# Kernel optimization log

Measured on AMD Instinct MI355X. Metric: run time of the kernel, lower is better.

Reference implementation:

```python
import jax, jax.numpy as jnp
import numpy as np

B, N, H, NH = 2, 2048, 1024, 16
HD = H // NH


def setup_inputs() -> dict:
    key = jax.random.key(0)
    ks = jax.random.split(key, 12)
    s = 0.02
    inp = {
        "q": jax.random.normal(ks[0], (B, N, H), jnp.float32),
        "k": jax.random.normal(ks[1], (B, N, H), jnp.float32),
        "v": jax.random.normal(ks[2], (B, N, H), jnp.float32),
        # causal mask, broadcast over batch and heads
        "mask": jnp.tril(jnp.ones((N, N), jnp.float32))[None, None, :, :],
        "Wq": jax.random.normal(ks[3], (H, H), jnp.float32) * s,
        "bq": jnp.zeros((H,), jnp.float32),
        "Wk": jax.random.normal(ks[4], (H, H), jnp.float32) * s,
        "bk": jnp.zeros((H,), jnp.float32),
        "Wv": jax.random.normal(ks[5], (H, H), jnp.float32) * s,
        "bv": jnp.zeros((H,), jnp.float32),
        "Wp": jax.random.normal(ks[6], (H, H), jnp.float32) * s,
        "bp": jnp.zeros((H,), jnp.float32),
    }
    return inp


def _split_heads(x):
    # [b, n, (h d)] -> [b, h, n, d]
    b, n, _ = x.shape
    return x.reshape(b, n, NH, HD).transpose(0, 2, 1, 3)


def reference(q, k, v, mask, Wq, bq, Wk, bk, Wv, bv, Wp, bp):
    Q = _split_heads(q @ Wq.T + bq)                      # [b,h,n,d]
    K = _split_heads(k @ Wk.T + bk)
    V = _split_heads(v @ Wv.T + bv)
    scores = jnp.einsum("bhnd,bhmd->bhnm", Q, K) / jnp.sqrt(jnp.float32(HD))
    scores = jnp.where(mask == 0, -jnp.inf, scores)
    attn = jax.nn.softmax(scores, axis=-1)
    out = jnp.einsum("bhnm,bhmd->bhnd", attn, V)         # [b,h,n,d]
    out = out.transpose(0, 2, 1, 3).reshape(q.shape[0], q.shape[1], H)
    # dropout is identity in eval mode
    return out @ Wp.T + bp
```

## Files before the change

kernel.cpp:

```cpp
#include <hip/hip_runtime.h>


typedef unsigned short ushortT;
typedef unsigned int uintT;
typedef __attribute__((ext_vector_type(8))) short short8;
typedef __attribute__((ext_vector_type(4))) float f32x4;

#define M_ROWS 4096
#define KDIM   1024
#define NDIM   1024
#define SEQ    2048
#define HDHEAD 64

__device__ __forceinline__ float bf2f(ushortT s) {
    union { unsigned u; float f; } v; v.u = ((unsigned)s) << 16; return v.f;
}
__device__ __forceinline__ ushortT f2bf(float x) {
    union { float f; unsigned u; } v; v.f = x;
    return (ushortT)((v.u + 0x7fffu + ((v.u >> 16) & 1u)) >> 16);
}

__device__ __forceinline__ bool detect_f32(const uintT* w) {
    int hits = 0;
#pragma unroll
    for (int i = 0; i < 16; ++i) {
        const unsigned e = (w[i] >> 7) & 0xffu;
        hits += (e >= 118u && e <= 131u) ? 1 : 0;
    }
    return hits < 8;
}

__device__ __forceinline__ short8 cvt8(const float* p) {
    f32x4 a = *(const f32x4*)p;
    f32x4 b = *(const f32x4*)(p + 4);
    short8 r;
    r[0] = (short)f2bf(a[0]); r[1] = (short)f2bf(a[1]);
    r[2] = (short)f2bf(a[2]); r[3] = (short)f2bf(a[3]);
    r[4] = (short)f2bf(b[0]); r[5] = (short)f2bf(b[1]);
    r[6] = (short)f2bf(b[2]); r[7] = (short)f2bf(b[3]);
    return r;
}

__device__ __forceinline__ void gl2lds16(const ushortT* g, ushortT* l) {
    __builtin_amdgcn_global_load_lds(
        (const __attribute__((address_space(1))) void*)g,
        (__attribute__((address_space(3))) void*)l,
        16, 0, 0);
}

__global__ __launch_bounds__(256) void convert_kernel(
    const void* __restrict__ q, const void* __restrict__ k, const void* __restrict__ v,
    const void* __restrict__ Wq, const void* __restrict__ Wk,
    const void* __restrict__ Wv, const void* __restrict__ Wp,
    const void* __restrict__ bq, const void* __restrict__ bk,
    const void* __restrict__ bv, const void* __restrict__ bp,
    ushortT* __restrict__ dst) {
    const bool f32m = detect_f32((const uintT*)q);
    const size_t u = (size_t)blockIdx.x * 256 + threadIdx.x;

    const void* src; size_t soff, doff;
    if (u < 1572864u) {
        const int seg = (int)(u >> 19);
        const size_t o = u & 524287u;
        src  = seg == 0 ? q : (seg == 1 ? k : v);
        soff = o * 8;
        doff = (size_t)seg * 4194304u + o * 8;
    } else if (u < 2097152u) {
        const size_t u2 = u - 1572864u;
        const int seg = (int)(u2 >> 17);
        const size_t o = u2 & 131071u;
        src  = seg == 0 ? Wq : (seg == 1 ? Wk : (seg == 2 ? Wv : Wp));
        soff = o * 8;
        doff = 12582912u + (size_t)seg * 1048576u + o * 8;
    } else {
        const size_t u3 = u - 2097152u;
        const int seg = (int)(u3 >> 7);
        const size_t o = u3 & 127u;
        src  = seg == 0 ? bq : (seg == 1 ? bk : (seg == 2 ? bv : bp));
        soff = o * 8;
        doff = 16777216u + (size_t)seg * 1024u + o * 8;
    }

    if (f32m)
        *(short8*)(dst + doff) = cvt8((const float*)src + soff);
    else
        *(short8*)(dst + doff) = *(const short8*)((const ushortT*)src + soff);
}

__device__ __forceinline__ void gemm_body(const void* __restrict__ Av,
                                          const void* __restrict__ Wv_,
                                          const void* __restrict__ biasv,
                                          void* __restrict__ Cv,
                                          bool a_f32, bool w_f32, bool c_f32) {
    __shared__ ushortT ldsA[128 * 32];
    __shared__ ushortT ldsB[128 * 32];

    const int tid  = threadIdx.x;
    const int lane = tid & 63;
    const int wid  = tid >> 6;
    const int bm   = blockIdx.x;
    const int bn   = blockIdx.y;
    const int wm   = wid >> 1;
    const int wn   = wid & 1;

    const int srow = lane >> 2;
    const int scol = (lane & 3) * 8;

    f32x4 acc[4][4];
#pragma unroll
    for (int i = 0; i < 4; ++i)
#pragma unroll
        for (int j = 0; j < 4; ++j) acc[i][j] = (f32x4){0.f, 0.f, 0.f, 0.f};

    const int fr   = lane & 15;
    const int quad = lane >> 4;

    for (int kt = 0; kt < KDIM / 32; ++kt) {
        const int k0 = kt * 32;
        if (!a_f32 && !w_f32) {
#pragma unroll
            for (int t = 0; t < 2; ++t) {
                const int chunk = wid * 2 + t;
                const size_t ra = (size_t)(bm * 128 + chunk * 16 + srow) * KDIM + k0 + scol;
                const size_t rw = (size_t)(bn * 128 + chunk * 16 + srow) * KDIM + k0 + scol;
                gl2lds16((const ushortT*)Av + ra, ldsA + chunk * 512);
                gl2lds16((const ushortT*)Wv_ + rw, ldsB + chunk * 512);
            }
        } else {
            short8 ta[2], tb[2];
#pragma unroll
            for (int t = 0; t < 2; ++t) {
                const int chunk = wid * 2 + t;
                const size_t ra = (size_t)(bm * 128 + chunk * 16 + srow) * KDIM + k0 + scol;
                const size_t rw = (size_t)(bn * 128 + chunk * 16 + srow) * KDIM + k0 + scol;
                ta[t] = a_f32 ? cvt8((const float*)Av + ra)
                              : *(const short8*)((const ushortT*)Av + ra);
                tb[t] = w_f32 ? cvt8((const float*)Wv_ + rw)
                              : *(const short8*)((const ushortT*)Wv_ + rw);
            }
#pragma unroll
            for (int t = 0; t < 2; ++t) {
                const int chunk = wid * 2 + t;
                *(short8*)(ldsA + chunk * 512 + lane * 8) = ta[t];
                *(short8*)(ldsB + chunk * 512 + lane * 8) = tb[t];
            }
        }
        __syncthreads();

        short8 aF[4], bF[4];
#pragma unroll
        for (int i = 0; i < 4; ++i)
            aF[i] = *(const short8*)(ldsA + (wm * 64 + i * 16 + fr) * 32 + quad * 8);
#pragma unroll
        for (int j = 0; j < 4; ++j)
            bF[j] = *(const short8*)(ldsB + (wn * 64 + j * 16 + fr) * 32 + quad * 8);
#pragma unroll
        for (int i = 0; i < 4; ++i)
#pragma unroll
            for (int j = 0; j < 4; ++j)
                acc[i][j] = __builtin_amdgcn_mfma_f32_16x16x32_bf16(aF[i], bF[j], acc[i][j], 0, 0, 0);
        __syncthreads();
    }

#pragma unroll
    for (int j = 0; j < 4; ++j) {
        const int col = bn * 128 + wn * 64 + j * 16 + fr;
        const float bv = w_f32 ? ((const float*)biasv)[col]
                               : bf2f(((const ushortT*)biasv)[col]);
#pragma unroll
        for (int i = 0; i < 4; ++i) {
            const int row0 = bm * 128 + wm * 64 + i * 16 + quad * 4;
#pragma unroll
            for (int r = 0; r < 4; ++r) {
                const float val = acc[i][j][r] + bv;
                if (c_f32)
                    ((float*)Cv)[(size_t)(row0 + r) * NDIM + col] = val;
                else
                    ((ushortT*)Cv)[(size_t)(row0 + r) * NDIM + col] = f2bf(val);
            }
        }
    }
}

__global__ __launch_bounds__(256, 2) void qkv_proj_kernel(
    const void* __restrict__ q, const void* __restrict__ k, const void* __restrict__ v,
    const void* __restrict__ Wq, const void* __restrict__ Wk, const void* __restrict__ Wv,
    const void* __restrict__ bq, const void* __restrict__ bk, const void* __restrict__ bv,
    ushortT* __restrict__ Qp, ushortT* __restrict__ Kp, ushortT* __restrict__ Vp) {
    const bool f32m = detect_f32((const uintT*)q);
    const void* A; const void* W; const void* bias; ushortT* C;
    if (blockIdx.z == 0)      { A = q; W = Wq; bias = bq; C = Qp; }
    else if (blockIdx.z == 1) { A = k; W = Wk; bias = bk; C = Kp; }
    else                      { A = v; W = Wv; bias = bv; C = Vp; }
    gemm_body(A, W, bias, (void*)C, f32m, f32m, false);
}

__global__ __launch_bounds__(256, 2) void out_proj_kernel(
    const ushortT* __restrict__ A, const void* __restrict__ W,
    const void* __restrict__ bias, void* __restrict__ C,
    const void* __restrict__ qdet) {
    const bool wf = detect_f32((const uintT*)W);
    const bool cf = detect_f32((const uintT*)qdet);
    gemm_body((const void*)A, W, bias, C, false, wf, cf);
}

__global__ __launch_bounds__(256, 2) void flash_attn_kernel(
    const ushortT* __restrict__ Qp, const ushortT* __restrict__ Kp,
    const ushortT* __restrict__ Vp, ushortT* __restrict__ Op) {
    __shared__ ushortT ldsK[2 * 64 * 40];
    __shared__ ushortT ldsV[64 * 72];
    __shared__ ushortT ldsP[4][16 * 72];

    const int tid  = threadIdx.x;
    const int lane = tid & 63;
    const int wid  = tid >> 6;
    const int fr   = lane & 15;
    const int quad = lane >> 4;

    const int pid = blockIdx.x;
    const int h   = blockIdx.y;
    const int b   = blockIdx.z;

    const size_t base = (size_t)b * SEQ * NDIM + (size_t)h * HDHEAD;
    const float scale = 0.125f;

    int ksst[2], keyloc[2];
#pragma unroll
    for (int t = 0; t < 2; ++t) {
        const int chunk = wid * 2 + t;
        ksst[t]   = chunk >> 2;
        keyloc[t] = (chunk & 3) * 16 + (lane >> 2);
    }
    const int c8 = (lane & 3) * 8;
    const int vj = lane;

    for (int half = 0; half < 2; ++half) {
        const int qb = (half == 0) ? pid : (31 - pid);
        const int q0 = qb * 64;
        const int nkv = qb + 1;

        short8 qf[2];
#pragma unroll
        for (int ks = 0; ks < 2; ++ks)
            qf[ks] = *(const short8*)(Qp + base + (size_t)(q0 + wid * 16 + fr) * NDIM + ks * 32 + quad * 8);

        f32x4 accO[4];
#pragma unroll
        for (int dt = 0; dt < 4; ++dt) accO[dt] = (f32x4){0.f, 0.f, 0.f, 0.f};
        float lsum[4];
#pragma unroll
        for (int r = 0; r < 4; ++r) lsum[r] = 0.f;

        short8 kreg[2], vreg[2];
#pragma unroll
        for (int t = 0; t < 2; ++t) {
            kreg[t] = *(const short8*)(Kp + base + (size_t)keyloc[t] * NDIM + ksst[t] * 32 + c8);
            vreg[t] = *(const short8*)(Vp + base + (size_t)vj * NDIM + (wid + t * 4) * 8);
        }

        for (int kt = 0; kt < nkv; ++kt) {
            __syncthreads();

#pragma unroll
            for (int t = 0; t < 2; ++t)
                *(short8*)(ldsK + ksst[t] * 2560 + keyloc[t] * 40 + c8) = kreg[t];
#pragma unroll
            for (int t = 0; t < 2; ++t) {
                const int d0 = (wid + t * 4) * 8;
                const ushortT* vs = (const ushortT*)&vreg[t];
#pragma unroll
                for (int i = 0; i < 8; ++i)
                    ldsV[(d0 + i) * 72 + vj] = vs[i];
            }

            if (kt + 1 < nkv) {
                const int kv1 = (kt + 1) * 64;
#pragma unroll
                for (int t = 0; t < 2; ++t) {
                    kreg[t] = *(const short8*)(Kp + base + (size_t)(kv1 + keyloc[t]) * NDIM + ksst[t] * 32 + c8);
                    vreg[t] = *(const short8*)(Vp + base + (size_t)(kv1 + vj) * NDIM + (wid + t * 4) * 8);
                }
            }
            __syncthreads();

            f32x4 s[4];
#pragma unroll
            for (int nt = 0; nt < 4; ++nt) {
                f32x4 a = (f32x4){0.f, 0.f, 0.f, 0.f};
#pragma unroll
                for (int ks = 0; ks < 2; ++ks) {
                    short8 kf = *(const short8*)(ldsK + ks * 2560 + (nt * 16 + fr) * 40 + quad * 8);
                    a = __builtin_amdgcn_mfma_f32_16x16x32_bf16(qf[ks], kf, a, 0, 0, 0);
                }
                s[nt] = a;
            }

            const int kv0 = kt * 64;
            const int qi = q0 + wid * 16 + quad * 4;
            if (kt == nkv - 1) {
#pragma unroll
                for (int nt = 0; nt < 4; ++nt) {
                    const int kj = kv0 + nt * 16 + fr;
#pragma unroll
                    for (int r = 0; r < 4; ++r) {
                        float vv = s[nt][r] * scale;
                        s[nt][r] = (kj > qi + r) ? -1e30f : vv;
                    }
                }
            } else {
#pragma unroll
                for (int nt = 0; nt < 4; ++nt)
#pragma unroll
                    for (int r = 0; r < 4; ++r) s[nt][r] *= scale;
            }

            ushortT* pbuf = ldsP[wid];
#pragma unroll
            for (int nt = 0; nt < 4; ++nt) {
#pragma unroll
                for (int r = 0; r < 4; ++r) {
                    const float p = __expf(fminf(s[nt][r], 30.f));
                    lsum[r] += p;
                    pbuf[(quad * 4 + r) * 72 + nt * 16 + fr] = f2bf(p);
                }
            }

            asm volatile("" ::: "memory");

#pragma unroll
            for (int ks = 0; ks < 2; ++ks) {
                short8 pf = *(const short8*)(pbuf + fr * 72 + ks * 32 + quad * 8);
#pragma unroll
                for (int dt = 0; dt < 4; ++dt) {
                    short8 vf = *(const short8*)(ldsV + (dt * 16 + fr) * 72 + ks * 32 + quad * 8);
                    accO[dt] = __builtin_amdgcn_mfma_f32_16x16x32_bf16(pf, vf, accO[dt], 0, 0, 0);
                }
            }
        }

#pragma unroll
        for (int r = 0; r < 4; ++r) {
#pragma unroll
            for (int off = 8; off >= 1; off >>= 1)
                lsum[r] += __shfl_xor(lsum[r], off, 64);
        }
#pragma unroll
        for (int dt = 0; dt < 4; ++dt) {
#pragma unroll
            for (int r = 0; r < 4; ++r) {
                const size_t row = (size_t)(q0 + wid * 16 + quad * 4 + r);
                Op[(size_t)b * SEQ * NDIM + row * NDIM + h * HDHEAD + dt * 16 + fr] =
                    f2bf(accO[dt][r] / lsum[r]);
            }
        }
    }
}

extern "C" void kernel_launch(void* const* d_in, const int* in_sizes, int n_in,
                              void* d_out, int out_size, void* d_ws, size_t ws_size,
                              hipStream_t stream) {
    const void* q  = d_in[0];
    const void* k  = d_in[1];
    const void* v  = d_in[2];
    const void* Wq = d_in[4];
    const void* bq = d_in[5];
    const void* Wk = d_in[6];
    const void* bk = d_in[7];
    const void* Wv = d_in[8];
    const void* bv = d_in[9];
    const void* Wp = d_in[10];
    const void* bp = d_in[11];

    dim3 blk(256);
    const size_t FAST_WS = 58728448;

    if (ws_size >= FAST_WS) {
        ushortT* cb   = (ushortT*)d_ws;
        ushortT* qb16 = cb;
        ushortT* kb16 = cb + 4194304u;
        ushortT* vb16 = cb + 8388608u;
        ushortT* Wqb  = cb + 12582912u;
        ushortT* Wkb  = cb + 13631488u;
        ushortT* Wvb  = cb + 14680064u;
        ushortT* Wpb  = cb + 15728640u;
        ushortT* bqb  = cb + 16777216u;
        ushortT* bkb  = cb + 16778240u;
        ushortT* bvb  = cb + 16779264u;
        ushortT* bpb  = cb + 16780288u;
        ushortT* Qp   = cb + 16781312u;
        ushortT* Kp   = Qp + 4194304u;
        ushortT* Vp   = Kp + 4194304u;
        ushortT* Op   = qb16;

        convert_kernel<<<dim3(8194), blk, 0, stream>>>(
            q, k, v, Wq, Wk, Wv, Wp, bq, bk, bv, bp, cb);
        qkv_proj_kernel<<<dim3(32, 8, 3), blk, 0, stream>>>(
            qb16, kb16, vb16, Wqb, Wkb, Wvb, bqb, bkb, bvb, Qp, Kp, Vp);
        flash_attn_kernel<<<dim3(16, 16, 2), blk, 0, stream>>>(Qp, Kp, Vp, Op);
        out_proj_kernel<<<dim3(32, 8), blk, 0, stream>>>(Op, Wpb, bpb, d_out, q);
    } else {
        ushortT* ws = (ushortT*)d_ws;
        ushortT* Qp = ws;
        ushortT* Kp = ws + (size_t)M_ROWS * NDIM;
        ushortT* Vp = ws + (size_t)2 * M_ROWS * NDIM;
        ushortT* Op = ws + (size_t)3 * M_ROWS * NDIM;

        qkv_proj_kernel<<<dim3(32, 8, 3), blk, 0, stream>>>(
            q, k, v, Wq, Wk, Wv, bq, bk, bv, Qp, Kp, Vp);
        flash_attn_kernel<<<dim3(16, 16, 2), blk, 0, stream>>>(Qp, Kp, Vp, Op);
        out_proj_kernel<<<dim3(32, 8), blk, 0, stream>>>(Op, Wp, bp, d_out, q);
    }
}
```

Measured before the change: 251.9 us.

## Store V transposed from projection, fold softmax scale into Q, deepen GEMM K-tile

The QKV projection now writes V in a head-major transposed layout [b,h,d,n], so the attention kernel can store V tiles into LDS with vector writes instead of eight scalar scatter stores per thread. The 1/sqrt(d) scale is applied in the Q projection epilogue, which removes the per-element multiply in attention. The GEMM K-step doubles to 64, halving the number of barrier pairs per tile. In exchange, the transposed V store is a strided scalar scatter in the projection epilogue, LDS per GEMM block doubles, and scaling Q before bf16 rounding slightly changes numerics.

```diff
diff --git a/kernel.cpp b/kernel.cpp
--- a/kernel.cpp
+++ b/kernel.cpp
@@ -91,9 +91,10 @@
                                           const void* __restrict__ Wv_,
                                           const void* __restrict__ biasv,
                                           void* __restrict__ Cv,
-                                          bool a_f32, bool w_f32, bool c_f32) {
-    __shared__ ushortT ldsA[128 * 32];
-    __shared__ ushortT ldsB[128 * 32];
+                                          bool a_f32, bool w_f32, bool c_f32,
+                                          float cscale, bool vt_store) {
+    __shared__ ushortT ldsA[128 * 64];
+    __shared__ ushortT ldsB[128 * 64];
 
     const int tid  = threadIdx.x;
     const int lane = tid & 63;
@@ -115,50 +116,57 @@
     const int fr   = lane & 15;
     const int quad = lane >> 4;
 
-    for (int kt = 0; kt < KDIM / 32; ++kt) {
-        const int k0 = kt * 32;
+    for (int kt = 0; kt < KDIM / 64; ++kt) {
+        const int k0 = kt * 64;
         if (!a_f32 && !w_f32) {
 #pragma unroll
-            for (int t = 0; t < 2; ++t) {
-                const int chunk = wid * 2 + t;
-                const size_t ra = (size_t)(bm * 128 + chunk * 16 + srow) * KDIM + k0 + scol;
-                const size_t rw = (size_t)(bn * 128 + chunk * 16 + srow) * KDIM + k0 + scol;
+            for (int t = 0; t < 4; ++t) {
+                const int chunk = wid * 4 + t;
+                const int kh  = chunk >> 3;
+                const int r16 = (chunk & 7) * 16;
+                const size_t ra = (size_t)(bm * 128 + r16 + srow) * KDIM + k0 + kh * 32 + scol;
+                const size_t rw = (size_t)(bn * 128 + r16 + srow) * KDIM + k0 + kh * 32 + scol;
                 gl2lds16((const ushortT*)Av + ra, ldsA + chunk * 512);
                 gl2lds16((const ushortT*)Wv_ + rw, ldsB + chunk * 512);
             }
         } else {
-            short8 ta[2], tb[2];
-#pragma unroll
-            for (int t = 0; t < 2; ++t) {
-                const int chunk = wid * 2 + t;
-                const size_t ra = (size_t)(bm * 128 + chunk * 16 + srow) * KDIM + k0 + scol;
-                const size_t rw = (size_t)(bn * 128 + chunk * 16 + srow) * KDIM + k0 + scol;
+            short8 ta[4], tb[4];
+#pragma unroll
+            for (int t = 0; t < 4; ++t) {
+                const int chunk = wid * 4 + t;
+                const int kh  = chunk >> 3;
+                const int r16 = (chunk & 7) * 16;
+                const size_t ra = (size_t)(bm * 128 + r16 + srow) * KDIM + k0 + kh * 32 + scol;
+                const size_t rw = (size_t)(bn * 128 + r16 + srow) * KDIM + k0 + kh * 32 + scol;
                 ta[t] = a_f32 ? cvt8((const float*)Av + ra)
                               : *(const short8*)((const ushortT*)Av + ra);
                 tb[t] = w_f32 ? cvt8((const float*)Wv_ + rw)
                               : *(const short8*)((const ushortT*)Wv_ + rw);
             }
 #pragma unroll
-            for (int t = 0; t < 2; ++t) {
-                const int chunk = wid * 2 + t;
+            for (int t = 0; t < 4; ++t) {
+                const int chunk = wid * 4 + t;
                 *(short8*)(ldsA + chunk * 512 + lane * 8) = ta[t];
                 *(short8*)(ldsB + chunk * 512 + lane * 8) = tb[t];
             }
         }
         __syncthreads();
 
-        short8 aF[4], bF[4];
-#pragma unroll
-        for (int i = 0; i < 4; ++i)
-            aF[i] = *(const short8*)(ldsA + (wm * 64 + i * 16 + fr) * 32 + quad * 8);
-#pragma unroll
-        for (int j = 0; j < 4; ++j)
-            bF[j] = *(const short8*)(ldsB + (wn * 64 + j * 16 + fr) * 32 + quad * 8);
-#pragma unroll
-        for (int i = 0; i < 4; ++i)
+#pragma unroll
+        for (int s = 0; s < 2; ++s) {
+            short8 aF[4], bF[4];
+#pragma unroll
+            for (int i = 0; i < 4; ++i)
+                aF[i] = *(const short8*)(ldsA + s * 4096 + (wm * 64 + i * 16 + fr) * 32 + quad * 8);
 #pragma unroll
             for (int j = 0; j < 4; ++j)
-                acc[i][j] = __builtin_amdgcn_mfma_f32_16x16x32_bf16(aF[i], bF[j], acc[i][j], 0, 0, 0);
+                bF[j] = *(const short8*)(ldsB + s * 4096 + (wn * 64 + j * 16 + fr) * 32 + quad * 8);
+#pragma unroll
+            for (int i = 0; i < 4; ++i)
+#pragma unroll
+                for (int j = 0; j < 4; ++j)
+                    acc[i][j] = __builtin_amdgcn_mfma_f32_16x16x32_bf16(aF[i], bF[j], acc[i][j], 0, 0, 0);
+        }
         __syncthreads();
     }
 
@@ -172,11 +180,17 @@
             const int row0 = bm * 128 + wm * 64 + i * 16 + quad * 4;
 #pragma unroll
             for (int r = 0; r < 4; ++r) {
-                const float val = acc[i][j][r] + bv;
-                if (c_f32)
-                    ((float*)Cv)[(size_t)(row0 + r) * NDIM + col] = val;
-                else
-                    ((ushortT*)Cv)[(size_t)(row0 + r) * NDIM + col] = f2bf(val);
+                const float val = (acc[i][j][r] + bv) * cscale;
+                const int row = row0 + r;
+                if (vt_store) {
+                    const int bb = row >> 11, n = row & 2047;
+                    const int hh = col >> 6,  d = col & 63;
+                    ((ushortT*)Cv)[(size_t)((bb * 16 + hh) * 64 + d) * SEQ + n] = f2bf(val);
+                } else if (c_f32) {
+                    ((float*)Cv)[(size_t)row * NDIM + col] = val;
+                } else {
+                    ((ushortT*)Cv)[(size_t)row * NDIM + col] = f2bf(val);
+                }
             }
         }
     }
@@ -186,13 +200,14 @@
     const void* __restrict__ q, const void* __restrict__ k, const void* __restrict__ v,
     const void* __restrict__ Wq, const void* __restrict__ Wk, const void* __restrict__ Wv,
     const void* __restrict__ bq, const void* __restrict__ bk, const void* __restrict__ bv,
-    ushortT* __restrict__ Qp, ushortT* __restrict__ Kp, ushortT* __restrict__ Vp) {
+    ushortT* __restrict__ Qp, ushortT* __restrict__ Kp, ushortT* __restrict__ Vt) {
     const bool f32m = detect_f32((const uintT*)q);
     const void* A; const void* W; const void* bias; ushortT* C;
-    if (blockIdx.z == 0)      { A = q; W = Wq; bias = bq; C = Qp; }
+    float cscale = 1.f; bool vt = false;
+    if (blockIdx.z == 0)      { A = q; W = Wq; bias = bq; C = Qp; cscale = 0.125f; }
     else if (blockIdx.z == 1) { A = k; W = Wk; bias = bk; C = Kp; }
-    else                      { A = v; W = Wv; bias = bv; C = Vp; }
-    gemm_body(A, W, bias, (void*)C, f32m, f32m, false);
+    else                      { A = v; W = Wv; bias = bv; C = Vt; vt = true; }
+    gemm_body(A, W, bias, (void*)C, f32m, f32m, false, cscale, vt);
 }
 
 __global__ __launch_bounds__(256, 2) void out_proj_kernel(
@@ -201,12 +216,12 @@
     const void* __restrict__ qdet) {
     const bool wf = detect_f32((const uintT*)W);
     const bool cf = detect_f32((const uintT*)qdet);
-    gemm_body((const void*)A, W, bias, C, false, wf, cf);
+    gemm_body((const void*)A, W, bias, C, false, wf, cf, 1.f, false);
 }
 
 __global__ __launch_bounds__(256, 2) void flash_attn_kernel(
     const ushortT* __restrict__ Qp, const ushortT* __restrict__ Kp,
-    const ushortT* __restrict__ Vp, ushortT* __restrict__ Op) {
+    const ushortT* __restrict__ Vt, ushortT* __restrict__ Op) {
     __shared__ ushortT ldsK[2 * 64 * 40];
     __shared__ ushortT ldsV[64 * 72];
     __shared__ ushortT ldsP[4][16 * 72];
@@ -221,8 +236,8 @@
     const int h   = blockIdx.y;
     const int b   = blockIdx.z;
 
-    const size_t base = (size_t)b * SEQ * NDIM + (size_t)h * HDHEAD;
-    const float scale = 0.125f;
+    const size_t base  = (size_t)b * SEQ * NDIM + (size_t)h * HDHEAD;
+    const size_t vtb   = (size_t)(b * 16 + h) * HDHEAD * SEQ;
 
     int ksst[2], keyloc[2];
 #pragma unroll
@@ -232,7 +247,8 @@
         keyloc[t] = (chunk & 3) * 16 + (lane >> 2);
     }
     const int c8 = (lane & 3) * 8;
-    const int vj = lane;
+    const int vd  = lane >> 3;
+    const int vk8 = (lane & 7) * 8;
 
     for (int half = 0; half < 2; ++half) {
         const int qb = (half == 0) ? pid : (31 - pid);
@@ -255,22 +271,18 @@
 #pragma unroll
         for (int t = 0; t < 2; ++t) {
             kreg[t] = *(const short8*)(Kp + base + (size_t)keyloc[t] * NDIM + ksst[t] * 32 + c8);
-            vreg[t] = *(const short8*)(Vp + base + (size_t)vj * NDIM + (wid + t * 4) * 8);
+            const int d = (wid * 2 + t) * 8 + vd;
+            vreg[t] = *(const short8*)(Vt + vtb + (size_t)d * SEQ + vk8);
         }
 
         for (int kt = 0; kt < nkv; ++kt) {
             __syncthreads();
 
 #pragma unroll
-            for (int t = 0; t < 2; ++t)
+            for (int t = 0; t < 2; ++t) {
                 *(short8*)(ldsK + ksst[t] * 2560 + keyloc[t] * 40 + c8) = kreg[t];
-#pragma unroll
-            for (int t = 0; t < 2; ++t) {
-                const int d0 = (wid + t * 4) * 8;
-                const ushortT* vs = (const ushortT*)&vreg[t];
-#pragma unroll
-                for (int i = 0; i < 8; ++i)
-                    ldsV[(d0 + i) * 72 + vj] = vs[i];
+                const int d = (wid * 2 + t) * 8 + vd;
+                *(short8*)(ldsV + d * 72 + vk8) = vreg[t];
             }
 
             if (kt + 1 < nkv) {
@@ -278,7 +290,8 @@
 #pragma unroll
                 for (int t = 0; t < 2; ++t) {
                     kreg[t] = *(const short8*)(Kp + base + (size_t)(kv1 + keyloc[t]) * NDIM + ksst[t] * 32 + c8);
-                    vreg[t] = *(const short8*)(Vp + base + (size_t)(kv1 + vj) * NDIM + (wid + t * 4) * 8);
+                    const int d = (wid * 2 + t) * 8 + vd;
+                    vreg[t] = *(const short8*)(Vt + vtb + (size_t)d * SEQ + kv1 + vk8);
                 }
             }
             __syncthreads();
@@ -302,16 +315,9 @@
                 for (int nt = 0; nt < 4; ++nt) {
                     const int kj = kv0 + nt * 16 + fr;
 #pragma unroll
-                    for (int r = 0; r < 4; ++r) {
-                        float vv = s[nt][r] * scale;
-                        s[nt][r] = (kj > qi + r) ? -1e30f : vv;
-                    }
-                }
-            } else {
-#pragma unroll
-                for (int nt = 0; nt < 4; ++nt)
-#pragma unroll
-                    for (int r = 0; r < 4; ++r) s[nt][r] *= scale;
+                    for (int r = 0; r < 4; ++r)
+                        s[nt][r] = (kj > qi + r) ? -1e30f : s[nt][r];
+                }
             }
 
             ushortT* pbuf = ldsP[wid];
@@ -389,25 +395,25 @@
         ushortT* bpb  = cb + 16780288u;
         ushortT* Qp   = cb + 16781312u;
         ushortT* Kp   = Qp + 4194304u;
-        ushortT* Vp   = Kp + 4194304u;
+        ushortT* Vt   = Kp + 4194304u;
         ushortT* Op   = qb16;
 
         convert_kernel<<<dim3(8194), blk, 0, stream>>>(
             q, k, v, Wq, Wk, Wv, Wp, bq, bk, bv, bp, cb);
         qkv_proj_kernel<<<dim3(32, 8, 3), blk, 0, stream>>>(
-            qb16, kb16, vb16, Wqb, Wkb, Wvb, bqb, bkb, bvb, Qp, Kp, Vp);
-        flash_attn_kernel<<<dim3(16, 16, 2), blk, 0, stream>>>(Qp, Kp, Vp, Op);
+            qb16, kb16, vb16, Wqb, Wkb, Wvb, bqb, bkb, bvb, Qp, Kp, Vt);
+        flash_attn_kernel<<<dim3(16, 16, 2), blk, 0, stream>>>(Qp, Kp, Vt, Op);
         out_proj_kernel<<<dim3(32, 8), blk, 0, stream>>>(Op, Wpb, bpb, d_out, q);
     } else {
         ushortT* ws = (ushortT*)d_ws;
         ushortT* Qp = ws;
         ushortT* Kp = ws + (size_t)M_ROWS * NDIM;
-        ushortT* Vp = ws + (size_t)2 * M_ROWS * NDIM;
+        ushortT* Vt = ws + (size_t)2 * M_ROWS * NDIM;
         ushortT* Op = ws + (size_t)3 * M_ROWS * NDIM;
 
         qkv_proj_kernel<<<dim3(32, 8, 3), blk, 0, stream>>>(
-            q, k, v, Wq, Wk, Wv, bq, bk, bv, Qp, Kp, Vp);
-        flash_attn_kernel<<<dim3(16, 16, 2), blk, 0, stream>>>(Qp, Kp, Vp, Op);
+            q, k, v, Wq, Wk, Wv, bq, bk, bv, Qp, Kp, Vt);
+        flash_attn_kernel<<<dim3(16, 16, 2), blk, 0, stream>>>(Qp, Kp, Vt, Op);
         out_proj_kernel<<<dim3(32, 8), blk, 0, stream>>>(Op, Wp, bp, d_out, q);
     }
 }
```

Result: faster. 242.6 us (-3.7%).
